# Performance work log

Hardware: AMD Instinct MI355X
Metric: run time of the kernel (lower is better)

The kernel has to match this reference:

```python
import jax, jax.numpy as jnp
import numpy as np

EPSILON = 0.001
PROXIMITY_THRESHOLD = 0.15


def setup_inputs() -> dict:
    key = jax.random.key(0)
    k1, k2, k3 = jax.random.split(key, 3)
    B, N, E = 8, 512, 4096
    node_positions = jax.random.uniform(k1, (B, N, 2), dtype=jnp.float32)
    adjacency = jax.random.normal(k2, (B, N, N), dtype=jnp.float32)
    edge_index = jax.random.randint(k3, (2, E), 0, B * N, dtype=jnp.int64)
    return {"node_positions": node_positions, "adjacency": adjacency, "edge_index": edge_index}


def _candidate_mask(pos, src, dst, batch, prox):
    # pos: (BN,2); src/dst/batch: (E,)
    p_src = pos[src]
    p_dst = pos[dst]
    mid = (p_src + p_dst) * 0.5                      # (E,2)
    half = jnp.linalg.norm(p_dst - p_src, axis=-1) * 0.5  # (E,)
    dist = jnp.linalg.norm(mid[:, None] - mid[None, :], axis=-1)  # (E,E)
    reach = half[:, None] + half[None, :] + prox
    E = src.shape[0]
    idx = jnp.arange(E)
    upper = idx[None, :] > idx[:, None]              # ei < ej
    same_batch = batch[:, None] == batch[None, :]
    shares = ((src[:, None] == src[None, :]) | (src[:, None] == dst[None, :])
              | (dst[:, None] == src[None, :]) | (dst[:, None] == dst[None, :]))
    return (dist < reach) & upper & same_batch & ~shares


def _segment_distance_dense(p_src, p_dst):
    # All-pairs closest-approach distance between segments i and j.
    d1 = p_dst - p_src                               # (E,2)
    sq = jnp.maximum((d1 * d1).sum(-1), 1e-12)       # (E,)
    a = sq[:, None]                                  # a_i
    e = sq[None, :]                                  # e_j
    b = d1 @ d1.T                                    # (E,E) d1_i . d1_j
    d1_dot_a1 = (d1 * p_src).sum(-1)                 # (E,) d1_k . a1_k
    c = d1_dot_a1[:, None] - d1 @ p_src.T            # d1_i . (a1_i - b1_j)
    f = p_src @ d1.T - d1_dot_a1[None, :]            # d1_j . (a1_i - b1_j)
    denom = jnp.maximum(a * e - b * b, 1e-12)
    s = (b * f - c * e) / denom
    t = (a * f - b * c) / denom
    s = jnp.clip(s, 0.0, 1.0)
    t = jnp.clip(t, 0.0, 1.0)
    t = jnp.clip((b * s + f) / e, 0.0, 1.0)
    s = jnp.clip((b * t - c) / a, 0.0, 1.0)
    closest_a = p_src[:, None, :] + s[..., None] * d1[:, None, :]   # (E,E,2)
    closest_b = p_src[None, :, :] + t[..., None] * d1[None, :, :]   # (E,E,2)
    return jnp.linalg.norm(closest_a - closest_b, axis=-1)          # (E,E)


def reference(node_positions, adjacency, edge_index):
    # adjacency is accepted (per the torch forward signature) but unused by this axiom.
    B, N, _ = node_positions.shape
    pos = node_positions.reshape(-1, 2)              # (B*N, 2)
    src = edge_index[0]
    dst = edge_index[1]
    batch = src // N                                 # (E,) batch membership per edge
    mask = jax.lax.stop_gradient(
        _candidate_mask(jax.lax.stop_gradient(pos), src, dst, batch, PROXIMITY_THRESHOLD))
    dmin = _segment_distance_dense(pos[src], pos[dst])  # (E,E)
    pair_loss = jax.nn.relu(EPSILON - dmin) * mask.astype(dmin.dtype)
    n_pairs = mask.sum()
    loss = pair_loss.sum() / jnp.maximum(n_pairs, 1).astype(dmin.dtype)
    violation_mask = mask & (pair_loss > 0)
    violation_scores = jax.lax.stop_gradient(pair_loss)
    return loss, violation_mask, violation_scores
```

## Files before the change

### kernel.cpp

```cpp
#include <hip/hip_runtime.h>


#define EDGES   4096
#define LOGE    12
#define EPS     0.001f
#define PROX    0.15f
#define NBUCKET 2048
#define ITILE   8
#define JBLK    512

__global__ __launch_bounds__(256) void edge_pre(
    const float2* __restrict__ pos,
    const int*    __restrict__ esrc,
    const int*    __restrict__ edst,
    float4* __restrict__ rec1, float4* __restrict__ rec2, float4* __restrict__ rec3)
{
#pragma clang fp contract(off)
    const int e = blockIdx.x * 256 + threadIdx.x;
    const int s = esrc[e], d = edst[e];
    const float2 a1 = pos[s], a2 = pos[d];
    const float d1x = a2.x - a1.x, d1y = a2.y - a1.y;
    const float midx = (a1.x + a2.x) * 0.5f, midy = (a1.y + a2.y) * 0.5f;
    const float half = sqrtf(d1x * d1x + d1y * d1y) * 0.5f;
    const float sq   = fmaxf(d1x * d1x + d1y * d1y, 1e-12f);
    const float dda  = d1x * a1.x + d1y * a1.y;
    rec1[e] = make_float4(a1.x, a1.y, d1x, d1y);
    rec2[e] = make_float4(midx, midy, half, dda);
    rec3[e] = make_float4(sq, __int_as_float(s), __int_as_float(d), 0.0f);
}

#define ZF_BLOCKS 2048
#define ZF_T      (ZF_BLOCKS * 256)
#define ZF_QUADS  8388607u
__global__ __launch_bounds__(256) void zero_fill(float* __restrict__ out)
{
    const unsigned g = blockIdx.x * 256 + threadIdx.x;
    float4* __restrict__ base = (float4*)(out + 4);
    const float4 z4 = make_float4(0.0f, 0.0f, 0.0f, 0.0f);
    #pragma unroll
    for (unsigned p = 0; p < 16; ++p) {
        const unsigned idx = g + p * (unsigned)ZF_T;
        if (idx < ZF_QUADS) base[idx] = z4;
    }
    if (g == 0) {
        out[1] = 0.0f; out[2] = 0.0f; out[3] = 0.0f;
        out[2 * EDGES * EDGES] = 0.0f;
    }
}

__global__ __launch_bounds__(256) void mask_seg(
    const float4* __restrict__ rec1, const float4* __restrict__ rec2,
    const float4* __restrict__ rec3,
    float*        __restrict__ out,
    float*        __restrict__ bsum,
    unsigned*     __restrict__ bcnt)
{
#pragma clang fp contract(off)
    const int ibase = blockIdx.y * ITILE;
    const int jbase = blockIdx.x * JBLK;
    const int tid   = threadIdx.x;

    if (jbase + JBLK - 1 <= ibase) return;

    float* __restrict__ o_mask  = out + 1;
    float* __restrict__ o_score = out + 1 + EDGES * EDGES;

    __shared__ unsigned lds_list[4][1024];
    const int wid  = tid >> 6, lane = tid & 63;
    const unsigned long long ltmask = (1ull << lane) - 1ull;

    const int j0 = jbase + tid;
    const int j1 = j0 + 256;
    const float4 r2j0 = rec2[j0], r3j0 = rec3[j0];
    const float4 r2j1 = rec2[j1], r3j1 = rec3[j1];
    const int sj0 = __float_as_int(r3j0.y), dj0 = __float_as_int(r3j0.z);
    const int sj1 = __float_as_int(r3j1.y), dj1 = __float_as_int(r3j1.z);

    unsigned wcount = 0;

    #pragma unroll
    for (int ii = 0; ii < ITILE; ++ii) {
        const int i = ibase + ii;
        const float4 r2i = rec2[i], r3i = rec3[i];
        const int si = __float_as_int(r3i.y), di = __float_as_int(r3i.z);

        {
            const float dmx = r2i.x - r2j0.x, dmy = r2i.y - r2j0.y;
            const float dist  = sqrtf(dmx * dmx + dmy * dmy);
            const float reach = r2i.z + r2j0.z + PROX;
            const bool shares = (si == sj0) | (si == dj0) | (di == sj0) | (di == dj0);
            const bool m = (dist < reach) & (j0 > i) & ((si >> 9) == (sj0 >> 9)) & (!shares);
            const unsigned long long b = __ballot(m);
            if (m) lds_list[wid][wcount + __popcll(b & ltmask)] = (unsigned)((i << LOGE) | j0);
            wcount += (unsigned)__popcll(b);
        }
        {
            const float dmx = r2i.x - r2j1.x, dmy = r2i.y - r2j1.y;
            const float dist  = sqrtf(dmx * dmx + dmy * dmy);
            const float reach = r2i.z + r2j1.z + PROX;
            const bool shares = (si == sj1) | (si == dj1) | (di == sj1) | (di == dj1);
            const bool m = (dist < reach) & (j1 > i) & ((si >> 9) == (sj1 >> 9)) & (!shares);
            const unsigned long long b = __ballot(m);
            if (m) lds_list[wid][wcount + __popcll(b & ltmask)] = (unsigned)((i << LOGE) | j1);
            wcount += (unsigned)__popcll(b);
        }
    }

    float vsum = 0.0f;
    for (unsigned u = lane; u < wcount; u += 64) {
        const unsigned k = lds_list[wid][u];
        const int i = (int)(k >> LOGE), j = (int)(k & (EDGES - 1));
        const float4 r1i = rec1[i], r2i = rec2[i], r3i = rec3[i];
        const float4 r1j = rec1[j], r2j = rec2[j], r3j = rec3[j];

        const float sqi = r3i.x, sqj = r3j.x;
        const float b = r1i.z * r1j.z + r1i.w * r1j.w;
        const float c = r2i.w - (r1i.z * r1j.x + r1i.w * r1j.y);
        const float f = (r1i.x * r1j.z + r1i.y * r1j.w) - r2j.w;
        const float denom = fmaxf(sqi * sqj - b * b, 1e-12f);

        float s = (b * f - c * sqj) / denom;
        s = fminf(fmaxf(s, 0.0f), 1.0f);
        const float t = fminf(fmaxf((b * s + f) / sqj, 0.0f), 1.0f);
        s = fminf(fmaxf((b * t - c) / sqi, 0.0f), 1.0f);

        const float cax = r1i.x + s * r1i.z, cay = r1i.y + s * r1i.w;
        const float cbx = r1j.x + t * r1j.z, cby = r1j.y + t * r1j.w;
        const float dx = cax - cbx, dy = cay - cby;
        const float dmin = sqrtf(dx * dx + dy * dy);

        const float pl = fmaxf(EPS - dmin, 0.0f);
        if (pl > 0.0f) {
            o_mask[k]  = 1.0f;
            o_score[k] = pl;
            vsum += pl;
        }
    }

    #pragma unroll
    for (int off = 32; off > 0; off >>= 1) vsum += __shfl_xor(vsum, off, 64);
    __shared__ float    ls[4];
    __shared__ unsigned lc[4];
    if (lane == 0) { ls[wid] = vsum; lc[wid] = wcount; }
    __syncthreads();
    if (tid == 0) {
        const float    s4 = ls[0] + ls[1] + ls[2] + ls[3];
        const unsigned c4 = lc[0] + lc[1] + lc[2] + lc[3];
        if (s4 != 0.0f || c4 != 0u) {
            const int bk = (blockIdx.y * 8 + blockIdx.x) & (NBUCKET - 1);
            atomicAdd(&bsum[bk], s4);
            atomicAdd(&bcnt[bk], c4);
        }
    }
}

__global__ __launch_bounds__(256) void finalize_kernel(
    const float* __restrict__ bsum, const unsigned* __restrict__ bcnt,
    float* __restrict__ out)
{
    float    s = 0.0f;
    unsigned c = 0u;
    for (int b = threadIdx.x; b < NBUCKET; b += 256) { s += bsum[b]; c += bcnt[b]; }
    #pragma unroll
    for (int off = 32; off > 0; off >>= 1) {
        s += __shfl_xor(s, off, 64);
        c += (unsigned)__shfl_xor((int)c, off, 64);
    }
    __shared__ float    ls[4];
    __shared__ unsigned lc[4];
    const int wid = threadIdx.x >> 6, lane = threadIdx.x & 63;
    if (lane == 0) { ls[wid] = s; lc[wid] = c; }
    __syncthreads();
    if (threadIdx.x == 0) {
        const float    st = ls[0] + ls[1] + ls[2] + ls[3];
        const unsigned ct = lc[0] + lc[1] + lc[2] + lc[3];
        const unsigned n  = ct > 1u ? ct : 1u;
        out[0] = st / (float)n;
    }
}

extern "C" void kernel_launch(void* const* d_in, const int* in_sizes, int n_in,
                              void* d_out, int out_size, void* d_ws, size_t ws_size,
                              hipStream_t stream) {
    const float2* pos  = (const float2*)d_in[0];
    const int*    esrc = (const int*)d_in[2];
    const int*    edst = esrc + EDGES;

    float*    out  = (float*)d_out;
    char*     ws   = (char*)d_ws;
    float*    bsum = (float*)ws;
    unsigned* bcnt = (unsigned*)(ws + NBUCKET * 4);
    float4*   rec1 = (float4*)(ws + 65536);
    float4*   rec2 = rec1 + EDGES;
    float4*   rec3 = rec2 + EDGES;

    hipMemsetAsync(d_ws, 0, NBUCKET * 8, stream);

    edge_pre<<<EDGES / 256, 256, 0, stream>>>(pos, esrc, edst, rec1, rec2, rec3);
    zero_fill<<<ZF_BLOCKS, 256, 0, stream>>>(out);
    dim3 grid(EDGES / JBLK, EDGES / ITILE);
    mask_seg<<<grid, 256, 0, stream>>>(rec1, rec2, rec3, out, bsum, bcnt);
    finalize_kernel<<<1, 256, 0, stream>>>(bsum, bcnt, out);
}
```

Baseline: 182.1 us.

## Bucket edges by batch and evaluate only same-batch pairs

Edges are counted per batch, and a prefix sum plus an atomic scatter reorder their records into contiguous per-batch segments. A new pair kernel, launched over a grid indexed by batch, tests only pairs within one batch. This drops the roughly 7/8 of the all-pairs candidate tests that the old mask kernel rejected on the same-batch check. It adds a scatter kernel and extra workspace, and it maps sorted indices back to original ones to keep the i<j ordering and the output positions.

```diff
diff --git a/kernel.cpp b/kernel.cpp
--- a/kernel.cpp
+++ b/kernel.cpp
@@ -6,14 +6,15 @@
 #define EPS     0.001f
 #define PROX    0.15f
 #define NBUCKET 2048
-#define ITILE   8
-#define JBLK    512
+#define ACHUNK  16
+#define MAXC    1024
 
 __global__ __launch_bounds__(256) void edge_pre(
     const float2* __restrict__ pos,
     const int*    __restrict__ esrc,
     const int*    __restrict__ edst,
-    float4* __restrict__ rec1, float4* __restrict__ rec2, float4* __restrict__ rec3)
+    float4* __restrict__ rec1, float4* __restrict__ rec2, float4* __restrict__ rec3,
+    unsigned* __restrict__ bcount)
 {
 #pragma clang fp contract(off)
     const int e = blockIdx.x * 256 + threadIdx.x;
@@ -27,14 +28,32 @@
     rec1[e] = make_float4(a1.x, a1.y, d1x, d1y);
     rec2[e] = make_float4(midx, midy, half, dda);
     rec3[e] = make_float4(sq, __int_as_float(s), __int_as_float(d), 0.0f);
+
+    const int bv   = s >> 9;
+    const int lane = threadIdx.x & 63;
+    #pragma unroll
+    for (int v = 0; v < 8; ++v) {
+        const unsigned long long mk = __ballot(bv == v);
+        if (mk && lane == (__ffsll((long long)mk) - 1))
+            atomicAdd(&bcount[v], (unsigned)__popcll(mk));
+    }
 }
 
 #define ZF_BLOCKS 2048
 #define ZF_T      (ZF_BLOCKS * 256)
 #define ZF_QUADS  8388607u
-__global__ __launch_bounds__(256) void zero_fill(float* __restrict__ out)
+__global__ __launch_bounds__(256) void zero_fill(
+    float* __restrict__ out,
+    const unsigned* __restrict__ bcount, unsigned* __restrict__ boffset)
 {
     const unsigned g = blockIdx.x * 256 + threadIdx.x;
+    if (g == 0) {
+        unsigned acc = 0;
+        #pragma unroll
+        for (int v = 0; v < 8; ++v) { boffset[v] = acc; acc += bcount[v]; }
+        out[1] = 0.0f; out[2] = 0.0f; out[3] = 0.0f;
+        out[2 * EDGES * EDGES] = 0.0f;
+    }
     float4* __restrict__ base = (float4*)(out + 4);
     const float4 z4 = make_float4(0.0f, 0.0f, 0.0f, 0.0f);
     #pragma unroll
@@ -42,112 +61,137 @@
         const unsigned idx = g + p * (unsigned)ZF_T;
         if (idx < ZF_QUADS) base[idx] = z4;
     }
-    if (g == 0) {
-        out[1] = 0.0f; out[2] = 0.0f; out[3] = 0.0f;
-        out[2 * EDGES * EDGES] = 0.0f;
-    }
-}
-
-__global__ __launch_bounds__(256) void mask_seg(
+}
+
+__global__ __launch_bounds__(256) void edge_scatter(
     const float4* __restrict__ rec1, const float4* __restrict__ rec2,
     const float4* __restrict__ rec3,
-    float*        __restrict__ out,
-    float*        __restrict__ bsum,
-    unsigned*     __restrict__ bcnt)
+    const unsigned* __restrict__ boffset, unsigned* __restrict__ bcursor,
+    float4* __restrict__ srec1, float4* __restrict__ srec2,
+    float4* __restrict__ srec3, unsigned* __restrict__ sorig)
+{
+    const int e    = blockIdx.x * 256 + threadIdx.x;
+    const int lane = threadIdx.x & 63;
+    const unsigned long long ltmask = (1ull << lane) - 1ull;
+    const float4 r3 = rec3[e];
+    const int bv = __float_as_int(r3.y) >> 9;
+
+    unsigned slot = 0;
+    #pragma unroll
+    for (int v = 0; v < 8; ++v) {
+        const unsigned long long mk = __ballot(bv == v);
+        if (mk) {
+            const int leader = __ffsll((long long)mk) - 1;
+            unsigned basev = 0;
+            if (lane == leader) basev = atomicAdd(&bcursor[v], (unsigned)__popcll(mk));
+            basev = (unsigned)__shfl((int)basev, leader, 64);
+            if (bv == v) slot = boffset[v] + basev + (unsigned)__popcll(mk & ltmask);
+        }
+    }
+    srec1[slot] = rec1[e];
+    srec2[slot] = rec2[e];
+    srec3[slot] = r3;
+    sorig[slot] = (unsigned)e;
+}
+
+__global__ __launch_bounds__(256) void pair_kernel(
+    const float4* __restrict__ srec1, const float4* __restrict__ srec2,
+    const float4* __restrict__ srec3, const unsigned* __restrict__ sorig,
+    const unsigned* __restrict__ bcount, const unsigned* __restrict__ boffset,
+    float* __restrict__ out,
+    float* __restrict__ bsum, unsigned* __restrict__ bcnt)
 {
 #pragma clang fp contract(off)
-    const int ibase = blockIdx.y * ITILE;
-    const int jbase = blockIdx.x * JBLK;
-    const int tid   = threadIdx.x;
-
-    if (jbase + JBLK - 1 <= ibase) return;
+    const int bz   = blockIdx.z;
+    const int cnt  = (int)bcount[bz];
+    const int off  = (int)boffset[bz];
+    const int abase = blockIdx.x * ACHUNK;
+    const int bbase = blockIdx.y * 256;
+    if (abase >= cnt || bbase >= cnt) return;
+    if (abase >= bbase + 256) return;
 
     float* __restrict__ o_mask  = out + 1;
     float* __restrict__ o_score = out + 1 + EDGES * EDGES;
 
-    __shared__ unsigned lds_list[4][1024];
-    const int wid  = tid >> 6, lane = tid & 63;
-    const unsigned long long ltmask = (1ull << lane) - 1ull;
-
-    const int j0 = jbase + tid;
-    const int j1 = j0 + 256;
-    const float4 r2j0 = rec2[j0], r3j0 = rec3[j0];
-    const float4 r2j1 = rec2[j1], r3j1 = rec3[j1];
-    const int sj0 = __float_as_int(r3j0.y), dj0 = __float_as_int(r3j0.z);
-    const int sj1 = __float_as_int(r3j1.y), dj1 = __float_as_int(r3j1.z);
-
-    unsigned wcount = 0;
-
-    #pragma unroll
-    for (int ii = 0; ii < ITILE; ++ii) {
-        const int i = ibase + ii;
-        const float4 r2i = rec2[i], r3i = rec3[i];
-        const int si = __float_as_int(r3i.y), di = __float_as_int(r3i.z);
-
-        {
-            const float dmx = r2i.x - r2j0.x, dmy = r2i.y - r2j0.y;
+    const int tid  = threadIdx.x;
+    const int bidx = bbase + tid;
+    const bool havb = bidx < cnt;
+
+    float4 br1, br2, br3; int ob = 0;
+    if (havb) {
+        br1 = srec1[off + bidx]; br2 = srec2[off + bidx]; br3 = srec3[off + bidx];
+        ob  = (int)sorig[off + bidx];
+    }
+    const int bs = havb ? __float_as_int(br3.y) : -1;
+    const int bd = havb ? __float_as_int(br3.z) : -1;
+
+    float vsum = 0.0f;
+    int   vcnt = 0;
+
+    const int aend = (abase + ACHUNK < cnt) ? abase + ACHUNK : cnt;
+    for (int aa = abase; aa < aend; ++aa) {
+        const int slotA = off + aa;
+        const float4 ar1 = srec1[slotA], ar2 = srec2[slotA], ar3 = srec3[slotA];
+        const int oa = (int)sorig[slotA];
+        const int as_ = __float_as_int(ar3.y), ad = __float_as_int(ar3.z);
+
+        const bool act = havb && (aa < bidx);
+        if (!__ballot(act)) continue;
+        if (act) {
+            const float dmx = ar2.x - br2.x, dmy = ar2.y - br2.y;
             const float dist  = sqrtf(dmx * dmx + dmy * dmy);
-            const float reach = r2i.z + r2j0.z + PROX;
-            const bool shares = (si == sj0) | (si == dj0) | (di == sj0) | (di == dj0);
-            const bool m = (dist < reach) & (j0 > i) & ((si >> 9) == (sj0 >> 9)) & (!shares);
-            const unsigned long long b = __ballot(m);
-            if (m) lds_list[wid][wcount + __popcll(b & ltmask)] = (unsigned)((i << LOGE) | j0);
-            wcount += (unsigned)__popcll(b);
+            const float reach = ar2.z + br2.z + PROX;
+            const bool shares = (as_ == bs) | (as_ == bd) | (ad == bs) | (ad == bd);
+            const bool m = (dist < reach) & (!shares);
+            vcnt += m ? 1 : 0;
+            if (m) {
+                const bool ai = oa < ob;
+                const float4 r1i = ai ? ar1 : br1, r2i = ai ? ar2 : br2, r3i = ai ? ar3 : br3;
+                const float4 r1j = ai ? br1 : ar1, r2j = ai ? br2 : ar2, r3j = ai ? br3 : ar3;
+
+                const float sqi = r3i.x, sqj = r3j.x;
+                const float b = r1i.z * r1j.z + r1i.w * r1j.w;
+                const float c = r2i.w - (r1i.z * r1j.x + r1i.w * r1j.y);
+                const float f = (r1i.x * r1j.z + r1i.y * r1j.w) - r2j.w;
+                const float denom = fmaxf(sqi * sqj - b * b, 1e-12f);
+
+                float s = (b * f - c * sqj) / denom;
+                s = fminf(fmaxf(s, 0.0f), 1.0f);
+                const float t = fminf(fmaxf((b * s + f) / sqj, 0.0f), 1.0f);
+                s = fminf(fmaxf((b * t - c) / sqi, 0.0f), 1.0f);
+
+                const float cax = r1i.x + s * r1i.z, cay = r1i.y + s * r1i.w;
+                const float cbx = r1j.x + t * r1j.z, cby = r1j.y + t * r1j.w;
+                const float dx = cax - cbx, dy = cay - cby;
+                const float dmin = sqrtf(dx * dx + dy * dy);
+
+                const float pl = fmaxf(EPS - dmin, 0.0f);
+                if (pl > 0.0f) {
+                    const int io = ai ? oa : ob, jo = ai ? ob : oa;
+                    const int k  = (io << LOGE) | jo;
+                    o_mask[k]  = 1.0f;
+                    o_score[k] = pl;
+                    vsum += pl;
+                }
+            }
         }
-        {
-            const float dmx = r2i.x - r2j1.x, dmy = r2i.y - r2j1.y;
-            const float dist  = sqrtf(dmx * dmx + dmy * dmy);
-            const float reach = r2i.z + r2j1.z + PROX;
-            const bool shares = (si == sj1) | (si == dj1) | (di == sj1) | (di == dj1);
-            const bool m = (dist < reach) & (j1 > i) & ((si >> 9) == (sj1 >> 9)) & (!shares);
-            const unsigned long long b = __ballot(m);
-            if (m) lds_list[wid][wcount + __popcll(b & ltmask)] = (unsigned)((i << LOGE) | j1);
-            wcount += (unsigned)__popcll(b);
-        }
-    }
-
-    float vsum = 0.0f;
-    for (unsigned u = lane; u < wcount; u += 64) {
-        const unsigned k = lds_list[wid][u];
-        const int i = (int)(k >> LOGE), j = (int)(k & (EDGES - 1));
-        const float4 r1i = rec1[i], r2i = rec2[i], r3i = rec3[i];
-        const float4 r1j = rec1[j], r2j = rec2[j], r3j = rec3[j];
-
-        const float sqi = r3i.x, sqj = r3j.x;
-        const float b = r1i.z * r1j.z + r1i.w * r1j.w;
-        const float c = r2i.w - (r1i.z * r1j.x + r1i.w * r1j.y);
-        const float f = (r1i.x * r1j.z + r1i.y * r1j.w) - r2j.w;
-        const float denom = fmaxf(sqi * sqj - b * b, 1e-12f);
-
-        float s = (b * f - c * sqj) / denom;
-        s = fminf(fmaxf(s, 0.0f), 1.0f);
-        const float t = fminf(fmaxf((b * s + f) / sqj, 0.0f), 1.0f);
-        s = fminf(fmaxf((b * t - c) / sqi, 0.0f), 1.0f);
-
-        const float cax = r1i.x + s * r1i.z, cay = r1i.y + s * r1i.w;
-        const float cbx = r1j.x + t * r1j.z, cby = r1j.y + t * r1j.w;
-        const float dx = cax - cbx, dy = cay - cby;
-        const float dmin = sqrtf(dx * dx + dy * dy);
-
-        const float pl = fmaxf(EPS - dmin, 0.0f);
-        if (pl > 0.0f) {
-            o_mask[k]  = 1.0f;
-            o_score[k] = pl;
-            vsum += pl;
-        }
-    }
-
-    #pragma unroll
-    for (int off = 32; off > 0; off >>= 1) vsum += __shfl_xor(vsum, off, 64);
+    }
+
+    #pragma unroll
+    for (int o = 32; o > 0; o >>= 1) {
+        vsum += __shfl_xor(vsum, o, 64);
+        vcnt += __shfl_xor(vcnt, o, 64);
+    }
     __shared__ float    ls[4];
     __shared__ unsigned lc[4];
-    if (lane == 0) { ls[wid] = vsum; lc[wid] = wcount; }
+    const int wid = tid >> 6, lane = tid & 63;
+    if (lane == 0) { ls[wid] = vsum; lc[wid] = (unsigned)vcnt; }
     __syncthreads();
     if (tid == 0) {
         const float    s4 = ls[0] + ls[1] + ls[2] + ls[3];
         const unsigned c4 = lc[0] + lc[1] + lc[2] + lc[3];
         if (s4 != 0.0f || c4 != 0u) {
-            const int bk = (blockIdx.y * 8 + blockIdx.x) & (NBUCKET - 1);
+            const int bk = (((blockIdx.z * gridDim.y + blockIdx.y) * gridDim.x) + blockIdx.x) & (NBUCKET - 1);
             atomicAdd(&bsum[bk], s4);
             atomicAdd(&bcnt[bk], c4);
         }
@@ -162,9 +206,9 @@
     unsigned c = 0u;
     for (int b = threadIdx.x; b < NBUCKET; b += 256) { s += bsum[b]; c += bcnt[b]; }
     #pragma unroll
-    for (int off = 32; off > 0; off >>= 1) {
-        s += __shfl_xor(s, off, 64);
-        c += (unsigned)__shfl_xor((int)c, off, 64);
+    for (int o = 32; o > 0; o >>= 1) {
+        s += __shfl_xor(s, o, 64);
+        c += (unsigned)__shfl_xor((int)c, o, 64);
     }
     __shared__ float    ls[4];
     __shared__ unsigned lc[4];
@@ -186,19 +230,29 @@
     const int*    esrc = (const int*)d_in[2];
     const int*    edst = esrc + EDGES;
 
-    float*    out  = (float*)d_out;
-    char*     ws   = (char*)d_ws;
-    float*    bsum = (float*)ws;
-    unsigned* bcnt = (unsigned*)(ws + NBUCKET * 4);
-    float4*   rec1 = (float4*)(ws + 65536);
-    float4*   rec2 = rec1 + EDGES;
-    float4*   rec3 = rec2 + EDGES;
-
-    hipMemsetAsync(d_ws, 0, NBUCKET * 8, stream);
-
-    edge_pre<<<EDGES / 256, 256, 0, stream>>>(pos, esrc, edst, rec1, rec2, rec3);
-    zero_fill<<<ZF_BLOCKS, 256, 0, stream>>>(out);
-    dim3 grid(EDGES / JBLK, EDGES / ITILE);
-    mask_seg<<<grid, 256, 0, stream>>>(rec1, rec2, rec3, out, bsum, bcnt);
+    float*    out     = (float*)d_out;
+    char*     ws      = (char*)d_ws;
+    float*    bsum    = (float*)ws;
+    unsigned* bcnt    = (unsigned*)(ws + 8192);
+    unsigned* bcount  = (unsigned*)(ws + 16384);
+    unsigned* boffset = (unsigned*)(ws + 16384 + 32);
+    unsigned* bcursor = (unsigned*)(ws + 16384 + 64);
+    float4*   rec1    = (float4*)(ws + 32768);
+    float4*   rec2    = rec1 + EDGES;
+    float4*   rec3    = rec2 + EDGES;
+    float4*   srec1   = rec3 + EDGES;
+    float4*   srec2   = srec1 + EDGES;
+    float4*   srec3   = srec2 + EDGES;
+    unsigned* sorig   = (unsigned*)(srec3 + EDGES);
+
+    hipMemsetAsync(d_ws, 0, 16384 + 96, stream);
+
+    edge_pre<<<EDGES / 256, 256, 0, stream>>>(pos, esrc, edst, rec1, rec2, rec3, bcount);
+    zero_fill<<<ZF_BLOCKS, 256, 0, stream>>>(out, bcount, boffset);
+    edge_scatter<<<EDGES / 256, 256, 0, stream>>>(rec1, rec2, rec3, boffset, bcursor,
+                                                  srec1, srec2, srec3, sorig);
+    dim3 grid(MAXC / ACHUNK, MAXC / 256, 8);
+    pair_kernel<<<grid, 256, 0, stream>>>(srec1, srec2, srec3, sorig,
+                                          bcount, boffset, out, bsum, bcnt);
     finalize_kernel<<<1, 256, 0, stream>>>(bsum, bcnt, out);
 }
```

Result: slower. 206.7 us (+13.5%).
